# Kernel tuning notes

Hardware: AMD Instinct MI355X
Metric: run time of the kernel (lower is better)

The kernel has to match this reference:

```python
import jax, jax.numpy as jnp
import numpy as np

HID = 50
IN_DIM = 20
OUT_DIM = 8


def lstm_cell(x, h, c, Wih, Whh, bih, bhh):
    # PyTorch LSTMCell: gates ordered i, f, g, o
    gates = x @ Wih.T + bih + h @ Whh.T + bhh  # [B, 4*HID]
    i, f, g, o = jnp.split(gates, 4, axis=-1)
    i = jax.nn.sigmoid(i)
    f = jax.nn.sigmoid(f)
    g = jnp.tanh(g)
    o = jax.nn.sigmoid(o)
    c_new = f * c + i * g
    h_new = o * jnp.tanh(c_new)
    return h_new, c_new


def setup_inputs() -> dict:
    key = jax.random.key(0)
    ks = jax.random.split(key, 16)
    s = 1.0 / np.sqrt(HID)
    u = lambda k, shape, bound: jax.random.uniform(k, shape, jnp.float32, -bound, bound)
    inp = {
        "x": jax.random.normal(ks[0], (512, 1024, IN_DIM), jnp.float32),
        "W1": u(ks[1], (HID, IN_DIM), 1.0 / np.sqrt(IN_DIM)),
        "b1": u(ks[2], (HID,), 1.0 / np.sqrt(IN_DIM)),
        "Wih1": u(ks[3], (4 * HID, HID), s), "Whh1": u(ks[4], (4 * HID, HID), s),
        "bih1": u(ks[5], (4 * HID,), s), "bhh1": u(ks[6], (4 * HID,), s),
        "Wih2": u(ks[7], (4 * HID, HID), s), "Whh2": u(ks[8], (4 * HID, HID), s),
        "bih2": u(ks[9], (4 * HID,), s), "bhh2": u(ks[10], (4 * HID,), s),
        "Wih3": u(ks[11], (4 * HID, HID), s), "Whh3": u(ks[12], (4 * HID, HID), s),
        "bih3": u(ks[13], (4 * HID,), s), "bhh3": u(ks[14], (4 * HID,), s),
        "W2": u(ks[15], (OUT_DIM, HID), s),
        "b2": jnp.zeros((OUT_DIM,), jnp.float32),
    }
    return inp


def reference(x, W1, b1, Wih1, Whh1, bih1, bhh1, Wih2, Whh2, bih2, bhh2,
              Wih3, Whh3, bih3, bhh3, W2, b2):
    B, T, _ = x.shape
    # Precompute the input projection for all timesteps (linear1)
    hid_all = x @ W1.T + b1  # [B, T, HID]
    z = jnp.zeros((B, HID), x.dtype)
    # carry replicates the original's (buggy) state handling:
    #   h3, c2 = lstm3(h2, (h3, c3)); c3 is never updated (stays zero)
    def step(carry, hid_t):
        h1, c1, h2, c2, h3, c3 = carry
        h1, c1 = lstm_cell(hid_t, h1, c1, Wih1, Whh1, bih1, bhh1)
        h2, c2 = lstm_cell(h1, h2, c2, Wih2, Whh2, bih2, bhh2)
        h3, c2 = lstm_cell(h2, h3, c3, Wih3, Whh3, bih3, bhh3)
        out = h3 @ W2.T + b2
        return (h1, c1, h2, c2, h3, c3), out

    _, outs = jax.lax.scan(step, (z, z, z, z, z, z),
                           jnp.swapaxes(hid_all, 0, 1))  # scan over time
    return jnp.swapaxes(outs, 0, 1)  # [B, T, OUT_DIM]
```

## Files before the change

### kernel.cpp

```cpp
#include <hip/hip_runtime.h>


#define T_SEQ 1024
#define HID   50
#define IN_DIM 20
#define OUT_DIM 8
#define KP   52
#define KP2  104

typedef float f32x2 __attribute__((ext_vector_type(2)));
typedef float f32x4 __attribute__((ext_vector_type(4)));

__device__ __forceinline__ void pkfma(f32x2& d, f32x2 a, f32x2 b) {
    asm("v_pk_fma_f32 %0, %1, %2, %0" : "+v"(d) : "v"(a), "v"(b));
}

__device__ __forceinline__ float sigm(float x) {
    return __builtin_amdgcn_rcpf(1.0f + __expf(-x));
}
__device__ __forceinline__ float tanh_f(float x) {
    return fmaf(2.0f, sigm(2.0f * x), -1.0f);
}

#define X0 0
#define H1 312
#define H2 520
#define H3 728
#define GB 936
#define SMSZ 2136

__global__ __launch_bounds__(768, 3) void lstm_net_kernel(
    const float* __restrict__ x,
    const float* __restrict__ W1,   const float* __restrict__ b1,
    const float* __restrict__ Wih1, const float* __restrict__ Whh1,
    const float* __restrict__ bih1, const float* __restrict__ bhh1,
    const float* __restrict__ Wih2, const float* __restrict__ Whh2,
    const float* __restrict__ bih2, const float* __restrict__ bhh2,
    const float* __restrict__ Wih3, const float* __restrict__ Whh3,
    const float* __restrict__ bih3, const float* __restrict__ bhh3,
    const float* __restrict__ W2,   const float* __restrict__ b2,
    float* __restrict__ out)
{
    __shared__ __align__(16) float sm[SMSZ];

    const int tid = threadIdx.x;
    const int b0  = blockIdx.x * 2;

    for (int i = tid; i < SMSZ; i += 768) sm[i] = 0.f;
    __syncthreads();

    f32x2 wp[52];
    float biasr = 0.f;
    int   lyr = 0, g = 0;
    float a2 = 1.f, cc = 0.f;
    int   ob = 0, ok = 0;
    int   pb = 0, pj = 0;
    f32x2 c1 = {0.f, 0.f};
    float xstage = 0.f;

    if (tid < 600) {
        lyr = tid / 200; g = tid % 200;
        const float* Wih = (lyr == 0) ? Wih1 : (lyr == 1 ? Wih2 : Wih3);
        const float* Whh = (lyr == 0) ? Whh1 : (lyr == 1 ? Whh2 : Whh3);
        const float* bi  = (lyr == 0) ? bih1 : (lyr == 1 ? bih2 : bih3);
        const float* bh  = (lyr == 0) ? bhh1 : (lyr == 1 ? bhh2 : bhh3);
        #pragma unroll
        for (int j = 0; j < 25; j++) {
            wp[j].x      = Wih[g * 50 + 2 * j];
            wp[j].y      = Wih[g * 50 + 2 * j + 1];
            wp[26 + j].x = Whh[g * 50 + 2 * j];
            wp[26 + j].y = Whh[g * 50 + 2 * j + 1];
        }
        wp[25] = (f32x2){0.f, 0.f};
        wp[51] = (f32x2){0.f, 0.f};
        biasr = bi[g] + bh[g];
        if (g >= 100 && g < 150) { a2 = 2.f; cc = -1.f; }
    } else if (tid >= 640 && tid < 656) {
        int idx = tid - 640; ob = idx >> 3; ok = idx & 7;
        #pragma unroll
        for (int j = 0; j < 25; j++) {
            wp[j].x = W2[ok * 50 + 2 * j];
            wp[j].y = W2[ok * 50 + 2 * j + 1];
        }
        wp[25] = (f32x2){0.f, 0.f};
        biasr = b2[ok];
    } else if (tid >= 656 && tid < 756) {
        int idx = tid - 656; pb = idx / 50; pj = idx % 50;
        #pragma unroll
        for (int j = 0; j < 10; j++) {
            wp[j].x = W1[pj * 20 + 2 * j];
            wp[j].y = W1[pj * 20 + 2 * j + 1];
        }
        biasr = b1[pj];
        const f32x4* xv = (const f32x4*)(x + ((size_t)(b0 + pb)) * T_SEQ * IN_DIM);
        f32x2 s0 = {0.f, 0.f}, s1 = {0.f, 0.f};
        #pragma unroll
        for (int k = 0; k < 5; k++) {
            f32x4 u = xv[k];
            pkfma(s0, wp[2 * k], u.lo);
            pkfma(s0, wp[2 * k + 1], u.hi);
        }
        #pragma unroll
        for (int k = 0; k < 5; k++) {
            f32x4 u = xv[5 + k];
            pkfma(s1, wp[2 * k], u.lo);
            pkfma(s1, wp[2 * k + 1], u.hi);
        }
        sm[X0 + 0 * KP2 + pb * KP + pj] = s0.x + s0.y + biasr;
        sm[X0 + 1 * KP2 + pb * KP + pj] = s1.x + s1.y + biasr;
    }
    __syncthreads();

    for (int s = 0; s < T_SEQ + 3; ++s) {
        const int p = s & 1, pm = p ^ 1, q3 = s % 3;

        if (tid < 600) {
            const int offA = (lyr == 0) ? (X0 + q3 * KP2)
                           : ((lyr == 1) ? (H1 + pm * KP2) : (H2 + p * KP2));
            const int offB = (lyr == 0) ? (H1 + pm * KP2)
                           : ((lyr == 1) ? (H2 + p * KP2) : (H3 + pm * KP2));
            const f32x4* A0 = (const f32x4*)(sm + offA);
            const f32x4* A1 = (const f32x4*)(sm + offA + KP);
            const f32x4* B0 = (const f32x4*)(sm + offB);
            const f32x4* B1 = (const f32x4*)(sm + offB + KP);
            f32x2 ac0 = {0.f, 0.f}, ac1 = {0.f, 0.f};
            f32x2 ac2 = {0.f, 0.f}, ac3 = {0.f, 0.f};
            #pragma unroll
            for (int k = 0; k < 13; k++) {
                f32x4 u0 = A0[k], u1 = A1[k];
                pkfma(ac0, wp[2 * k],     u0.lo);
                pkfma(ac1, wp[2 * k + 1], u0.hi);
                pkfma(ac2, wp[2 * k],     u1.lo);
                pkfma(ac3, wp[2 * k + 1], u1.hi);
            }
            #pragma unroll
            for (int k = 0; k < 13; k++) {
                f32x4 u0 = B0[k], u1 = B1[k];
                pkfma(ac0, wp[26 + 2 * k],     u0.lo);
                pkfma(ac1, wp[26 + 2 * k + 1], u0.hi);
                pkfma(ac2, wp[26 + 2 * k],     u1.lo);
                pkfma(ac3, wp[26 + 2 * k + 1], u1.hi);
            }
            const float px_ = ac0.x + ac0.y + ac1.x + ac1.y + biasr;
            const float py_ = ac2.x + ac2.y + ac3.x + ac3.y + biasr;
            f32x2 r;
            r.x = fmaf(a2, sigm(a2 * px_), cc);
            r.y = fmaf(a2, sigm(a2 * py_), cc);
            ((f32x2*)(sm + GB))[lyr * 200 + g] = r;
        } else if (tid >= 640 && tid < 656) {
            if (s >= 3) {
                const int t = s - 3;
                const f32x4* hv = (const f32x4*)(sm + H3 + pm * KP2 + ob * KP);
                f32x2 ac = {0.f, 0.f}, acb = {0.f, 0.f};
                #pragma unroll
                for (int k = 0; k < 13; k++) {
                    f32x4 u = hv[k];
                    pkfma(ac,  wp[2 * k],     u.lo);
                    pkfma(acb, wp[2 * k + 1], u.hi);
                }
                out[((size_t)(b0 + ob) * T_SEQ + t) * OUT_DIM + ok]
                    = ac.x + ac.y + acb.x + acb.y + biasr;
            }
        } else if (tid >= 656 && tid < 756) {
            if (s + 2 < T_SEQ) {
                const f32x4* xv = (const f32x4*)
                    (x + (((size_t)(b0 + pb)) * T_SEQ + (s + 2)) * IN_DIM);
                f32x2 ac = {0.f, 0.f};
                #pragma unroll
                for (int k = 0; k < 5; k++) {
                    f32x4 u = xv[k];
                    pkfma(ac, wp[2 * k],     u.lo);
                    pkfma(ac, wp[2 * k + 1], u.hi);
                }
                xstage = ac.x + ac.y + biasr;
            }
        }
        __syncthreads();

        if (tid < 50) {
            if (s < T_SEQ) {
                const f32x2* gb = (const f32x2*)(sm + GB);
                f32x2 gi = gb[tid],       gf = gb[50 + tid];
                f32x2 gg = gb[100 + tid], go = gb[150 + tid];
                c1.x = fmaf(gf.x, c1.x, gi.x * gg.x);
                c1.y = fmaf(gf.y, c1.y, gi.y * gg.y);
                sm[H1 + p * KP2 + tid]      = go.x * tanh_f(c1.x);
                sm[H1 + p * KP2 + KP + tid] = go.y * tanh_f(c1.y);
            }
        } else if (tid >= 64 && tid < 114) {
            const int j = tid - 64;
            const f32x2* gb = (const f32x2*)(sm + GB);
            f32x2 cn3 = {0.f, 0.f};
            if (s >= 2 && s <= T_SEQ + 1) {
                f32x2 gi = gb[400 + j], gg = gb[500 + j], go = gb[550 + j];
                cn3.x = gi.x * gg.x;
                cn3.y = gi.y * gg.y;
                sm[H3 + p * KP2 + j]      = go.x * tanh_f(cn3.x);
                sm[H3 + p * KP2 + KP + j] = go.y * tanh_f(cn3.y);
            }
            if (s >= 1 && s <= T_SEQ) {
                f32x2 gi = gb[200 + j], gf = gb[250 + j];
                f32x2 gg = gb[300 + j], go = gb[350 + j];
                f32x2 c2n;
                c2n.x = fmaf(gf.x, cn3.x, gi.x * gg.x);
                c2n.y = fmaf(gf.y, cn3.y, gi.y * gg.y);
                sm[H2 + pm * KP2 + j]      = go.x * tanh_f(c2n.x);
                sm[H2 + pm * KP2 + KP + j] = go.y * tanh_f(c2n.y);
            }
        } else if (tid >= 656 && tid < 756) {
            if (s + 2 < T_SEQ) {
                sm[X0 + ((s + 2) % 3) * KP2 + pb * KP + pj] = xstage;
            }
        }
        __syncthreads();
    }
}

extern "C" void kernel_launch(void* const* d_in, const int* in_sizes, int n_in,
                              void* d_out, int out_size, void* d_ws, size_t ws_size,
                              hipStream_t stream) {
    const float* x    = (const float*)d_in[0];
    const float* W1   = (const float*)d_in[1];
    const float* b1   = (const float*)d_in[2];
    const float* Wih1 = (const float*)d_in[3];
    const float* Whh1 = (const float*)d_in[4];
    const float* bih1 = (const float*)d_in[5];
    const float* bhh1 = (const float*)d_in[6];
    const float* Wih2 = (const float*)d_in[7];
    const float* Whh2 = (const float*)d_in[8];
    const float* bih2 = (const float*)d_in[9];
    const float* bhh2 = (const float*)d_in[10];
    const float* Wih3 = (const float*)d_in[11];
    const float* Whh3 = (const float*)d_in[12];
    const float* bih3 = (const float*)d_in[13];
    const float* bhh3 = (const float*)d_in[14];
    const float* W2   = (const float*)d_in[15];
    const float* b2   = (const float*)d_in[16];
    float* out = (float*)d_out;

    dim3 grid(256), block(768);
    lstm_net_kernel<<<grid, block, 0, stream>>>(
        x, W1, b1, Wih1, Whh1, bih1, bhh1, Wih2, Whh2, bih2, bhh2,
        Wih3, Whh3, bih3, bhh3, W2, b2, out);
}
```

Measured before the change: 1.791 ms.

## Combine LSTM gates in registers via ds_swizzle, dropping one barrier per step

Each step now ends with a single __syncthreads instead of two. Threads are regrouped so the four gates of each hidden unit (and the layer-2 and layer-3 partners) sit in adjacent lanes, and the gate values are combined with ds_swizzle lane exchanges rather than a shared-memory gate buffer. The cell and hidden updates happen in the same phase as the gate matvec. The x-projection threads are reordered to load one step further ahead, which adds an extra prefetch stage. This removes one barrier and the shared-memory round trip from the serial recurrence, at the cost of more complex lane mapping and extra swizzle instructions.

```diff
diff --git a/kernel.cpp b/kernel.cpp
--- a/kernel.cpp
+++ b/kernel.cpp
@@ -8,26 +8,30 @@
 #define KP   52
 #define KP2  104
 
-typedef float f32x2 __attribute__((ext_vector_type(2)));
-typedef float f32x4 __attribute__((ext_vector_type(4)));
-
-__device__ __forceinline__ void pkfma(f32x2& d, f32x2 a, f32x2 b) {
-    asm("v_pk_fma_f32 %0, %1, %2, %0" : "+v"(d) : "v"(a), "v"(b));
-}
-
-__device__ __forceinline__ float sigm(float x) {
-    return __builtin_amdgcn_rcpf(1.0f + __expf(-x));
-}
-__device__ __forceinline__ float tanh_f(float x) {
-    return fmaf(2.0f, sigm(2.0f * x), -1.0f);
-}
-
-#define X0 0
 #define H1 312
 #define H2 520
 #define H3 728
-#define GB 936
-#define SMSZ 2136
+#define SMSZ 936
+
+typedef float f32x2 __attribute__((ext_vector_type(2)));
+typedef float f32x4 __attribute__((ext_vector_type(4)));
+
+__device__ __forceinline__ void pkfma(f32x2& d, f32x2 a, f32x2 b) {
+    asm("v_pk_fma_f32 %0, %1, %2, %0" : "+v"(d) : "v"(a), "v"(b));
+}
+__device__ __forceinline__ float sigm(float x) {
+    return __builtin_amdgcn_rcpf(1.0f + __expf(-x));
+}
+__device__ __forceinline__ float tanh_f(float x) {
+    return fmaf(2.0f, sigm(2.0f * x), -1.0f);
+}
+template <int IMM>
+__device__ __forceinline__ f32x2 swz2(f32x2 v) {
+    f32x2 r;
+    r.x = __int_as_float(__builtin_amdgcn_ds_swizzle(__float_as_int(v.x), IMM));
+    r.y = __int_as_float(__builtin_amdgcn_ds_swizzle(__float_as_int(v.y), IMM));
+    return r;
+}
 
 __global__ __launch_bounds__(768, 3) void lstm_net_kernel(
     const float* __restrict__ x,
@@ -51,63 +55,90 @@
 
     f32x2 wp[52];
     float biasr = 0.f;
-    int   lyr = 0, g = 0;
     float a2 = 1.f, cc = 0.f;
-    int   ob = 0, ok = 0;
-    int   pb = 0, pj = 0;
-    f32x2 c1 = {0.f, 0.f};
-    float xstage = 0.f;
+    int   dly = 0, cA = 0, cB = 1;
+    int   comb = 0, j = 0;
+    bool  alive = true;
+    int   ob = 0, ok = 0, pj = 0;
+    f32x2 c1  = {0.f, 0.f};
+    f32x2 xst = {0.f, 0.f};
 
     if (tid < 600) {
-        lyr = tid / 200; g = tid % 200;
-        const float* Wih = (lyr == 0) ? Wih1 : (lyr == 1 ? Wih2 : Wih3);
-        const float* Whh = (lyr == 0) ? Whh1 : (lyr == 1 ? Whh2 : Whh3);
-        const float* bi  = (lyr == 0) ? bih1 : (lyr == 1 ? bih2 : bih3);
-        const float* bh  = (lyr == 0) ? bhh1 : (lyr == 1 ? bhh2 : bhh3);
-        #pragma unroll
-        for (int j = 0; j < 25; j++) {
-            wp[j].x      = Wih[g * 50 + 2 * j];
-            wp[j].y      = Wih[g * 50 + 2 * j + 1];
-            wp[26 + j].x = Whh[g * 50 + 2 * j];
-            wp[26 + j].y = Whh[g * 50 + 2 * j + 1];
+        const float *Wih, *Whh, *bi, *bh;
+        int row, r;
+        if (tid < 400) {
+            const int grp = tid >> 3;  r = tid & 7;  j = grp;
+            if (r < 4) {
+                dly = 1; cA = 1; cB = 2;
+                Wih = Wih2; Whh = Whh2; bi = bih2; bh = bhh2;
+                row = (r == 0) ? grp : (r == 1) ? 100 + grp
+                    : (r == 2) ? 50 + grp : 150 + grp;
+                if (r == 1) { a2 = 2.f; cc = -1.f; }
+                if (r == 2) comb = 2;
+            } else {
+                const int rr = r - 4;
+                dly = 2; cA = 2; cB = 3;
+                Wih = Wih3; Whh = Whh3; bi = bih3; bh = bhh3;
+                row = (rr == 0) ? grp : (rr == 1) ? 100 + grp : 150 + grp;
+                if (rr == 1) { a2 = 2.f; cc = -1.f; }
+                if (rr == 2) comb = 3;
+                alive = (r != 7);
+            }
+        } else {
+            const int q = (tid - 400) >> 2;  r = tid & 3;  j = q;
+            dly = 0; cA = 0; cB = 1;
+            Wih = Wih1; Whh = Whh1; bi = bih1; bh = bhh1;
+            row = (r == 0) ? q : (r == 1) ? 100 + q
+                : (r == 2) ? 50 + q : 150 + q;
+            if (r == 1) { a2 = 2.f; cc = -1.f; }
+            if (r == 2) comb = 1;
+        }
+        #pragma unroll
+        for (int k = 0; k < 25; k++) {
+            wp[k].x      = Wih[row * 50 + 2 * k];
+            wp[k].y      = Wih[row * 50 + 2 * k + 1];
+            wp[26 + k].x = Whh[row * 50 + 2 * k];
+            wp[26 + k].y = Whh[row * 50 + 2 * k + 1];
         }
         wp[25] = (f32x2){0.f, 0.f};
         wp[51] = (f32x2){0.f, 0.f};
-        biasr = bi[g] + bh[g];
-        if (g >= 100 && g < 150) { a2 = 2.f; cc = -1.f; }
+        biasr = bi[row] + bh[row];
     } else if (tid >= 640 && tid < 656) {
-        int idx = tid - 640; ob = idx >> 3; ok = idx & 7;
-        #pragma unroll
-        for (int j = 0; j < 25; j++) {
-            wp[j].x = W2[ok * 50 + 2 * j];
-            wp[j].y = W2[ok * 50 + 2 * j + 1];
+        const int idx = tid - 640; ob = idx >> 3; ok = idx & 7;
+        #pragma unroll
+        for (int k = 0; k < 25; k++) {
+            wp[k].x = W2[ok * 50 + 2 * k];
+            wp[k].y = W2[ok * 50 + 2 * k + 1];
         }
         wp[25] = (f32x2){0.f, 0.f};
         biasr = b2[ok];
-    } else if (tid >= 656 && tid < 756) {
-        int idx = tid - 656; pb = idx / 50; pj = idx % 50;
-        #pragma unroll
-        for (int j = 0; j < 10; j++) {
-            wp[j].x = W1[pj * 20 + 2 * j];
-            wp[j].y = W1[pj * 20 + 2 * j + 1];
+    } else if (tid >= 704 && tid < 754) {
+        pj = tid - 704;
+        #pragma unroll
+        for (int k = 0; k < 10; k++) {
+            wp[k].x = W1[pj * 20 + 2 * k];
+            wp[k].y = W1[pj * 20 + 2 * k + 1];
         }
         biasr = b1[pj];
-        const f32x4* xv = (const f32x4*)(x + ((size_t)(b0 + pb)) * T_SEQ * IN_DIM);
-        f32x2 s0 = {0.f, 0.f}, s1 = {0.f, 0.f};
-        #pragma unroll
-        for (int k = 0; k < 5; k++) {
-            f32x4 u = xv[k];
-            pkfma(s0, wp[2 * k], u.lo);
-            pkfma(s0, wp[2 * k + 1], u.hi);
-        }
-        #pragma unroll
-        for (int k = 0; k < 5; k++) {
-            f32x4 u = xv[5 + k];
-            pkfma(s1, wp[2 * k], u.lo);
-            pkfma(s1, wp[2 * k + 1], u.hi);
-        }
-        sm[X0 + 0 * KP2 + pb * KP + pj] = s0.x + s0.y + biasr;
-        sm[X0 + 1 * KP2 + pb * KP + pj] = s1.x + s1.y + biasr;
+        #pragma unroll
+        for (int t = 0; t < 3; ++t) {
+            const f32x4* xv0 = (const f32x4*)(x + ((size_t)b0 * T_SEQ + t) * IN_DIM);
+            const f32x4* xv1 = (const f32x4*)(x + ((size_t)(b0 + 1) * T_SEQ + t) * IN_DIM);
+            f32x2 aX = {0.f, 0.f}, aY = {0.f, 0.f};
+            #pragma unroll
+            for (int k = 0; k < 5; k++) {
+                f32x4 u = xv0[k];
+                pkfma(aX, wp[2 * k], u.lo); pkfma(aX, wp[2 * k + 1], u.hi);
+            }
+            #pragma unroll
+            for (int k = 0; k < 5; k++) {
+                f32x4 u = xv1[k];
+                pkfma(aY, wp[2 * k], u.lo); pkfma(aY, wp[2 * k + 1], u.hi);
+            }
+            const float h0 = aX.x + aX.y + biasr, h1v = aY.x + aY.y + biasr;
+            if (t < 2) { sm[t * KP2 + pj] = h0; sm[t * KP2 + KP + pj] = h1v; }
+            else       { xst.x = h0; xst.y = h1v; }
+        }
     }
     __syncthreads();
 
@@ -115,10 +146,12 @@
         const int p = s & 1, pm = p ^ 1, q3 = s % 3;
 
         if (tid < 600) {
-            const int offA = (lyr == 0) ? (X0 + q3 * KP2)
-                           : ((lyr == 1) ? (H1 + pm * KP2) : (H2 + p * KP2));
-            const int offB = (lyr == 0) ? (H1 + pm * KP2)
-                           : ((lyr == 1) ? (H2 + p * KP2) : (H3 + pm * KP2));
+            const int vX  = q3 * KP2;
+            const int vH1 = H1 + pm * KP2;
+            const int vH2 = H2 + p  * KP2;
+            const int vH3 = H3 + pm * KP2;
+            const int offA = (cA == 0) ? vX  : (cA == 1 ? vH1 : vH2);
+            const int offB = (cB == 1) ? vH1 : (cB == 2 ? vH2 : vH3);
             const f32x4* A0 = (const f32x4*)(sm + offA);
             const f32x4* A1 = (const f32x4*)(sm + offA + KP);
             const f32x4* B0 = (const f32x4*)(sm + offB);
@@ -141,75 +174,71 @@
                 pkfma(ac2, wp[26 + 2 * k],     u1.lo);
                 pkfma(ac3, wp[26 + 2 * k + 1], u1.hi);
             }
-            const float px_ = ac0.x + ac0.y + ac1.x + ac1.y + biasr;
-            const float py_ = ac2.x + ac2.y + ac3.x + ac3.y + biasr;
-            f32x2 r;
-            r.x = fmaf(a2, sigm(a2 * px_), cc);
-            r.y = fmaf(a2, sigm(a2 * py_), cc);
-            ((f32x2*)(sm + GB))[lyr * 200 + g] = r;
+            const float sx = ac0.x + ac0.y + ac1.x + ac1.y + biasr;
+            const float sy = ac2.x + ac2.y + ac3.x + ac3.y + biasr;
+            const bool valid = alive && ((unsigned)(s - dly) < (unsigned)T_SEQ);
+            f32x2 a;
+            a.x = valid ? fmaf(a2, sigm(a2 * sx), cc) : 0.f;
+            a.y = valid ? fmaf(a2, sigm(a2 * sy), cc) : 0.f;
+
+            f32x2 t1 = swz2<0x80B1>(a);
+            f32x2 v2 = a * t1;
+            f32x2 t2 = swz2<0x804E>(v2);
+            f32x2 t3 = {0.f, 0.f};
+            if (tid < 400) t3 = swz2<0x101F>(t2);
+
+            if (comb == 1) {
+                c1.x = fmaf(a.x, c1.x, t2.x);
+                c1.y = fmaf(a.y, c1.y, t2.y);
+                sm[H1 + p * KP2 + j]      = t1.x * tanh_f(c1.x);
+                sm[H1 + p * KP2 + KP + j] = t1.y * tanh_f(c1.y);
+            } else if (comb == 2) {
+                const float cx = fmaf(a.x, t3.x, t2.x);
+                const float cy = fmaf(a.y, t3.y, t2.y);
+                sm[H2 + pm * KP2 + j]      = t1.x * tanh_f(cx);
+                sm[H2 + pm * KP2 + KP + j] = t1.y * tanh_f(cy);
+            } else if (comb == 3) {
+                sm[H3 + p * KP2 + j]      = a.x * tanh_f(t2.x);
+                sm[H3 + p * KP2 + KP + j] = a.y * tanh_f(t2.y);
+            }
         } else if (tid >= 640 && tid < 656) {
             if (s >= 3) {
                 const int t = s - 3;
                 const f32x4* hv = (const f32x4*)(sm + H3 + pm * KP2 + ob * KP);
-                f32x2 ac = {0.f, 0.f}, acb = {0.f, 0.f};
+                f32x2 e0 = {0.f, 0.f}, e1 = {0.f, 0.f};
                 #pragma unroll
                 for (int k = 0; k < 13; k++) {
                     f32x4 u = hv[k];
-                    pkfma(ac,  wp[2 * k],     u.lo);
-                    pkfma(acb, wp[2 * k + 1], u.hi);
+                    pkfma(e0, wp[2 * k],     u.lo);
+                    pkfma(e1, wp[2 * k + 1], u.hi);
                 }
                 out[((size_t)(b0 + ob) * T_SEQ + t) * OUT_DIM + ok]
-                    = ac.x + ac.y + acb.x + acb.y + biasr;
-            }
-        } else if (tid >= 656 && tid < 756) {
+                    = e0.x + e0.y + e1.x + e1.y + biasr;
+            }
+        } else if (tid >= 704 && tid < 754) {
+            const int sl = (s + 2) % 3;
             if (s + 2 < T_SEQ) {
-                const f32x4* xv = (const f32x4*)
-                    (x + (((size_t)(b0 + pb)) * T_SEQ + (s + 2)) * IN_DIM);
-                f32x2 ac = {0.f, 0.f};
+                sm[sl * KP2 + pj]      = xst.x;
+                sm[sl * KP2 + KP + pj] = xst.y;
+            }
+            if (s + 3 < T_SEQ) {
+                const f32x4* xv0 = (const f32x4*)
+                    (x + ((size_t)b0 * T_SEQ + (s + 3)) * IN_DIM);
+                const f32x4* xv1 = (const f32x4*)
+                    (x + ((size_t)(b0 + 1) * T_SEQ + (s + 3)) * IN_DIM);
+                f32x2 aX = {0.f, 0.f}, aY = {0.f, 0.f};
                 #pragma unroll
                 for (int k = 0; k < 5; k++) {
-                    f32x4 u = xv[k];
-                    pkfma(ac, wp[2 * k],     u.lo);
-                    pkfma(ac, wp[2 * k + 1], u.hi);
+                    f32x4 u = xv0[k];
+                    pkfma(aX, wp[2 * k], u.lo); pkfma(aX, wp[2 * k + 1], u.hi);
                 }
-                xstage = ac.x + ac.y + biasr;
-            }
-        }
-        __syncthreads();
-
-        if (tid < 50) {
-            if (s < T_SEQ) {
-                const f32x2* gb = (const f32x2*)(sm + GB);
-                f32x2 gi = gb[tid],       gf = gb[50 + tid];
-                f32x2 gg = gb[100 + tid], go = gb[150 + tid];
-                c1.x = fmaf(gf.x, c1.x, gi.x * gg.x);
-                c1.y = fmaf(gf.y, c1.y, gi.y * gg.y);
-                sm[H1 + p * KP2 + tid]      = go.x * tanh_f(c1.x);
-                sm[H1 + p * KP2 + KP + tid] = go.y * tanh_f(c1.y);
-            }
-        } else if (tid >= 64 && tid < 114) {
-            const int j = tid - 64;
-            const f32x2* gb = (const f32x2*)(sm + GB);
-            f32x2 cn3 = {0.f, 0.f};
-            if (s >= 2 && s <= T_SEQ + 1) {
-                f32x2 gi = gb[400 + j], gg = gb[500 + j], go = gb[550 + j];
-                cn3.x = gi.x * gg.x;
-                cn3.y = gi.y * gg.y;
-                sm[H3 + p * KP2 + j]      = go.x * tanh_f(cn3.x);
-                sm[H3 + p * KP2 + KP + j] = go.y * tanh_f(cn3.y);
-            }
-            if (s >= 1 && s <= T_SEQ) {
-                f32x2 gi = gb[200 + j], gf = gb[250 + j];
-                f32x2 gg = gb[300 + j], go = gb[350 + j];
-                f32x2 c2n;
-                c2n.x = fmaf(gf.x, cn3.x, gi.x * gg.x);
-                c2n.y = fmaf(gf.y, cn3.y, gi.y * gg.y);
-                sm[H2 + pm * KP2 + j]      = go.x * tanh_f(c2n.x);
-                sm[H2 + pm * KP2 + KP + j] = go.y * tanh_f(c2n.y);
-            }
-        } else if (tid >= 656 && tid < 756) {
-            if (s + 2 < T_SEQ) {
-                sm[X0 + ((s + 2) % 3) * KP2 + pb * KP + pj] = xstage;
+                #pragma unroll
+                for (int k = 0; k < 5; k++) {
+                    f32x4 u = xv1[k];
+                    pkfma(aY, wp[2 * k], u.lo); pkfma(aY, wp[2 * k + 1], u.hi);
+                }
+                xst.x = aX.x + aX.y + biasr;
+                xst.y = aY.x + aY.y + biasr;
             }
         }
         __syncthreads();
```

Measured after the change: 1.739 ms. 1.03x faster.
